# Performance work log

Measured on AMD Instinct MI355X. Metric: run time of the kernel, lower is better.

The kernel has to match this reference:

```python
import jax, jax.numpy as jnp
import numpy as np

B, T, H, W, C = 2, 8, 64, 64, 256
HEADS = 8
WS = 8


def setup_inputs() -> dict:
    key = jax.random.key(0)
    k1, k2, k3 = jax.random.split(key, 3)
    x = jax.random.normal(k1, (B, T, H, W, C), dtype=jnp.float32)
    qkv_w = jax.random.normal(k2, (C, 3 * C), dtype=jnp.float32) * (C ** -0.5)
    proj_w = jax.random.normal(k3, (C, C), dtype=jnp.float32) * (C ** -0.5)
    proj_b = jnp.zeros((C,), dtype=jnp.float32)
    return {"x": x, "qkv_w": qkv_w, "proj_w": proj_w, "proj_b": proj_b}


def reference(x, qkv_w, proj_w, proj_b):
    b, t, h, w, c = x.shape
    hn, wn = h // WS, w // WS
    dh = c // HEADS
    scale = dh ** -0.5
    # window partition: (B,T,H,W,C) -> (B*hn*wn, T*WS*WS, C)
    xw = x.reshape(b, t, hn, WS, wn, WS, c)
    xw = jnp.transpose(xw, (0, 2, 4, 1, 3, 5, 6)).reshape(-1, t * WS * WS, c)
    bw, n, _ = xw.shape
    qkv = (xw @ qkv_w).reshape(bw, n, 3, HEADS, dh)
    qkv = jnp.transpose(qkv, (2, 0, 3, 1, 4))  # (3, Bw, heads, N, dh)
    q, k, v = qkv[0], qkv[1], qkv[2]
    attn = jax.nn.softmax(jnp.einsum("bhnd,bhmd->bhnm", q, k) * scale, axis=-1)
    out = jnp.einsum("bhnm,bhmd->bhnd", attn, v)
    out = jnp.transpose(out, (0, 2, 1, 3)).reshape(bw, n, c)
    out = out @ proj_w + proj_b
    # window reverse
    out = out.reshape(b, hn, wn, t, WS, WS, c)
    out = jnp.transpose(out, (0, 3, 1, 4, 2, 5, 6)).reshape(b, t, h, w, c)
    return out
```

## Files before the change

kernel.cpp:

```cpp
#include <hip/hip_runtime.h>


typedef __bf16 bf16x8 __attribute__((ext_vector_type(8)));
typedef float f32x4 __attribute__((ext_vector_type(4)));

#define NTOK 512
#define DH 32
#define CDIM 256
#define C3 768

__device__ __forceinline__ unsigned short f2b(float f) {
  unsigned u = __builtin_bit_cast(unsigned, f);
  unsigned r = u + 0x7fffu + ((u >> 16) & 1u);
  return (unsigned short)(r >> 16);
}

__global__ void k_prep(const float* __restrict__ qkv_w, const float* __restrict__ proj_w,
                       unsigned short* __restrict__ wqT, unsigned short* __restrict__ wpT) {
  const float QS = 0.2550540254f;
  int idx = blockIdx.x * 256 + threadIdx.x;
  int stride = gridDim.x * 256;
  for (int i = idx; i < C3 * CDIM; i += stride) {
    int n = i >> 8, kk = i & 255;
    float f = qkv_w[kk * C3 + n];
    if (n < 256) f *= QS;
    wqT[i] = f2b(f);
  }
  for (int i = idx; i < CDIM * CDIM; i += stride) {
    int n = i >> 8, kk = i & 255;
    wpT[i] = f2b(proj_w[kk * CDIM + n]);
  }
}

__global__ __launch_bounds__(256, 2) void k_qkv(
    const float* __restrict__ x, const unsigned short* __restrict__ wqT,
    unsigned short* __restrict__ qo, unsigned short* __restrict__ ko,
    unsigned short* __restrict__ vo) {
  extern __shared__ char smem[];
  unsigned short (*As)[264] = (unsigned short (*)[264])smem;
  unsigned short (*Bs)[40]  = (unsigned short (*)[40])(smem + 128 * 264 * 2);
  int tid = threadIdx.x;
  int mtile = blockIdx.x;
  int bw = mtile >> 2;
  int n0 = (mtile & 3) << 7;
  int bb = bw >> 6, hi = (bw >> 3) & 7, wi = bw & 7;

  {
    int row = tid >> 1;
    int n = n0 + row;
    int tt = n >> 6, ii = (n >> 3) & 7, jj = n & 7;
    const float* src = x + ((((long)(bb * 8 + tt)) * 64 + (hi * 8 + ii)) * 64 + (wi * 8 + jj)) * 256;
    int fb = (tid & 1) * 4;
#pragma unroll
    for (int u = 0; u < 32; ++u) {
      int f = fb + u * 8;
      float4 d = *(const float4*)(src + f);
      __bf16 h0 = (__bf16)d.x, h1 = (__bf16)d.y, h2 = (__bf16)d.z, h3 = (__bf16)d.w;
      __bf16* dst = (__bf16*)&As[row][f];
      dst[0] = h0; dst[1] = h1; dst[2] = h2; dst[3] = h3;
    }
  }
  __syncthreads();

  int wid = tid >> 6, lane = tid & 63;
  int lg = lane >> 4, lr = lane & 15;
  int wr = wid >> 1, wc = wid & 1;

  for (int nt = 0; nt < 6; ++nt) {
    f32x4 acc[4][4];
#pragma unroll
    for (int a = 0; a < 4; ++a)
#pragma unroll
      for (int b2 = 0; b2 < 4; ++b2) acc[a][b2] = (f32x4){0.f, 0.f, 0.f, 0.f};

    for (int kk = 0; kk < 256; kk += 32) {
      __syncthreads();
      {
        int brow = tid >> 1, bh2 = tid & 1;
        const uint4* bs = (const uint4*)(wqT + ((long)(nt * 128 + brow)) * 256 + kk + bh2 * 16);
        uint4 b0 = bs[0], b1 = bs[1];
        *(uint4*)&Bs[brow][bh2 * 16] = b0;
        *(uint4*)&Bs[brow][bh2 * 16 + 8] = b1;
      }
      __syncthreads();
      bf16x8 af[4], bfr[4];
#pragma unroll
      for (int mi = 0; mi < 4; ++mi)
        af[mi] = *(const bf16x8*)&As[wr * 64 + mi * 16 + lr][kk + lg * 8];
#pragma unroll
      for (int ni = 0; ni < 4; ++ni)
        bfr[ni] = *(const bf16x8*)&Bs[wc * 64 + ni * 16 + lr][lg * 8];
#pragma unroll
      for (int mi = 0; mi < 4; ++mi)
#pragma unroll
        for (int ni = 0; ni < 4; ++ni)
          acc[mi][ni] = __builtin_amdgcn_mfma_f32_16x16x32_bf16(af[mi], bfr[ni], acc[mi][ni], 0, 0, 0);
    }
#pragma unroll
    for (int ni = 0; ni < 4; ++ni) {
      int c = nt * 128 + wc * 64 + ni * 16 + lr;
      int which = c >> 8, head = (c >> 5) & 7, d = c & 31;
      unsigned short* dst = (which == 0) ? qo : ((which == 1) ? ko : vo);
      long base = ((long)(bw * 8 + head)) * NTOK * DH + d;
#pragma unroll
      for (int mi = 0; mi < 4; ++mi) {
        int nloc = n0 + wr * 64 + mi * 16 + lg * 4;
#pragma unroll
        for (int r = 0; r < 4; ++r) {
          __bf16 hv = (__bf16)acc[mi][ni][r];
          dst[base + (long)(nloc + r) * DH] = __builtin_bit_cast(unsigned short, hv);
        }
      }
    }
  }
}

#define VTOFF 40960
#define POFF 74240
__global__ __launch_bounds__(256, 2) void k_attn(
    const unsigned short* __restrict__ qg0, const unsigned short* __restrict__ kg0,
    const unsigned short* __restrict__ vg0, unsigned short* __restrict__ og) {
  extern __shared__ char smem[];
  int bh = blockIdx.x;
  int tid = threadIdx.x;
  const unsigned short* qg = qg0 + (long)bh * NTOK * DH;
  const unsigned short* kg = kg0 + (long)bh * NTOK * DH;
  const unsigned short* vg = vg0 + (long)bh * NTOK * DH;

#pragma unroll
  for (int i2 = 0; i2 < 8; ++i2) {
    int ci = tid + i2 * 256;
    uint4 dd = *(const uint4*)(kg + ci * 8);
    int n = ci >> 2, h = ci & 3;
    *(uint4*)(smem + n * 80 + h * 16) = dd;
  }
  {
    const uint4* vs = (const uint4*)(vg + tid * 64);
    unsigned r0[16], r1[16];
    *(uint4*)&r0[0] = vs[0]; *(uint4*)&r0[4] = vs[1]; *(uint4*)&r0[8] = vs[2]; *(uint4*)&r0[12] = vs[3];
    *(uint4*)&r1[0] = vs[4]; *(uint4*)&r1[4] = vs[5]; *(uint4*)&r1[8] = vs[6]; *(uint4*)&r1[12] = vs[7];
#pragma unroll
    for (int d = 0; d < 32; ++d) {
      unsigned lo  = (r0[d >> 1] >> ((d & 1) * 16)) & 0xffffu;
      unsigned hi2 = (r1[d >> 1] >> ((d & 1) * 16)) & 0xffffu;
      *(unsigned*)(smem + VTOFF + d * 1040 + tid * 4) = lo | (hi2 << 16);
    }
  }
  __syncthreads();

  int wid = tid >> 6, lane = tid & 63;
  int lg = lane >> 4, lr = lane & 15;
  char* Pb = smem + POFF + wid * 1280;
  unsigned short* ob = og + (long)bh * NTOK * DH;
  const f32x4 zf = {0.f, 0.f, 0.f, 0.f};

  for (int pass = 0; pass < 4; ++pass) {
    int qA = pass * 128 + wid * 32;
    bf16x8 qf0 = *(const bf16x8*)(qg + (qA + lr) * DH + lg * 8);
    bf16x8 qf1 = *(const bf16x8*)(qg + (qA + 16 + lr) * DH + lg * 8);
    f32x4 o00 = zf, o01 = zf, o10 = zf, o11 = zf;
    float m0 = -1e30f, m1 = -1e30f, sum0 = 0.f, sum1 = 0.f;

    for (int ch = 0; ch < 4; ++ch) {
      f32x4 s0[8], s1[8];
#pragma unroll
      for (int t = 0; t < 8; ++t) {
        bf16x8 kf = *(const bf16x8*)(smem + ((ch * 8 + t) * 16 + lr) * 80 + lg * 16);
        s0[t] = __builtin_amdgcn_mfma_f32_16x16x32_bf16(kf, qf0, zf, 0, 0, 0);
        s1[t] = __builtin_amdgcn_mfma_f32_16x16x32_bf16(kf, qf1, zf, 0, 0, 0);
      }
      float mc0 = -1e30f, mc1 = -1e30f;
#pragma unroll
      for (int t = 0; t < 8; ++t)
#pragma unroll
        for (int r = 0; r < 4; ++r) {
          mc0 = fmaxf(mc0, s0[t][r]);
          mc1 = fmaxf(mc1, s1[t][r]);
        }
      mc0 = fmaxf(mc0, __shfl_xor(mc0, 16, 64));
      mc0 = fmaxf(mc0, __shfl_xor(mc0, 32, 64));
      mc1 = fmaxf(mc1, __shfl_xor(mc1, 16, 64));
      mc1 = fmaxf(mc1, __shfl_xor(mc1, 32, 64));
      float nm0 = fmaxf(m0, mc0), nm1 = fmaxf(m1, mc1);
      float sc0 = __builtin_amdgcn_exp2f(m0 - nm0);
      float sc1 = __builtin_amdgcn_exp2f(m1 - nm1);
      m0 = nm0; m1 = nm1;
      float ps0 = 0.f, ps1 = 0.f;
#pragma unroll
      for (int t = 0; t < 8; ++t)
#pragma unroll
        for (int r = 0; r < 4; ++r) {
          float p0 = __builtin_amdgcn_exp2f(s0[t][r] - nm0);
          float p1 = __builtin_amdgcn_exp2f(s1[t][r] - nm1);
          s0[t][r] = p0; s1[t][r] = p1;
          ps0 += p0; ps1 += p1;
        }
      ps0 += __shfl_xor(ps0, 16, 64);
      ps0 += __shfl_xor(ps0, 32, 64);
      ps1 += __shfl_xor(ps1, 16, 64);
      ps1 += __shfl_xor(ps1, 32, 64);
      sum0 = sum0 * sc0 + ps0;
      sum1 = sum1 * sc1 + ps1;
#pragma unroll
      for (int r = 0; r < 4; ++r) {
        float so0 = __shfl(sc0, lg * 4 + r, 64);
        float so1 = __shfl(sc1, lg * 4 + r, 64);
        o00[r] *= so0; o01[r] *= so0;
        o10[r] *= so1; o11[r] *= so1;
      }
#pragma unroll
      for (int mcl = 0; mcl < 4; ++mcl) {
        int mg = ch * 4 + mcl;
        bf16x8 vf0 = *(const bf16x8*)(smem + VTOFF + (lr) * 1040 + mg * 64 + lg * 16);
        bf16x8 vf1 = *(const bf16x8*)(smem + VTOFF + (16 + lr) * 1040 + mg * 64 + lg * 16);
#pragma unroll
        for (int u = 0; u < 2; ++u) {
          int t = mcl * 2 + u;
          __bf16* pw = (__bf16*)(Pb + lr * 80 + u * 32 + lg * 8);
          pw[0] = (__bf16)s0[t][0]; pw[1] = (__bf16)s0[t][1];
          pw[2] = (__bf16)s0[t][2]; pw[3] = (__bf16)s0[t][3];
        }
        bf16x8 pf0 = *(const bf16x8*)(Pb + lr * 80 + lg * 16);
        o00 = __builtin_amdgcn_mfma_f32_16x16x32_bf16(pf0, vf0, o00, 0, 0, 0);
        o01 = __builtin_amdgcn_mfma_f32_16x16x32_bf16(pf0, vf1, o01, 0, 0, 0);
#pragma unroll
        for (int u = 0; u < 2; ++u) {
          int t = mcl * 2 + u;
          __bf16* pw = (__bf16*)(Pb + lr * 80 + u * 32 + lg * 8);
          pw[0] = (__bf16)s1[t][0]; pw[1] = (__bf16)s1[t][1];
          pw[2] = (__bf16)s1[t][2]; pw[3] = (__bf16)s1[t][3];
        }
        bf16x8 pf1 = *(const bf16x8*)(Pb + lr * 80 + lg * 16);
        o10 = __builtin_amdgcn_mfma_f32_16x16x32_bf16(pf1, vf0, o10, 0, 0, 0);
        o11 = __builtin_amdgcn_mfma_f32_16x16x32_bf16(pf1, vf1, o11, 0, 0, 0);
      }
    }

    float rcp0 = 1.0f / sum0, rcp1 = 1.0f / sum1;
#pragma unroll
    for (int r = 0; r < 4; ++r) {
      float rr0 = __shfl(rcp0, lg * 4 + r, 64);
      int rowb = (lg * 4 + r) * 80;
      *(__bf16*)(Pb + rowb + lr * 2)      = (__bf16)(o00[r] * rr0);
      *(__bf16*)(Pb + rowb + 32 + lr * 2) = (__bf16)(o01[r] * rr0);
    }
    {
      int row = lane >> 2, qq = lane & 3;
      uint4 d0 = *(const uint4*)(Pb + row * 80 + qq * 16);
      *(uint4*)(ob + ((long)(qA + row)) * DH + qq * 8) = d0;
    }
#pragma unroll
    for (int r = 0; r < 4; ++r) {
      float rr1 = __shfl(rcp1, lg * 4 + r, 64);
      int rowb = (lg * 4 + r) * 80;
      *(__bf16*)(Pb + rowb + lr * 2)      = (__bf16)(o10[r] * rr1);
      *(__bf16*)(Pb + rowb + 32 + lr * 2) = (__bf16)(o11[r] * rr1);
    }
    {
      int row = lane >> 2, qq = lane & 3;
      uint4 d1 = *(const uint4*)(Pb + row * 80 + qq * 16);
      *(uint4*)(ob + ((long)(qA + 16 + row)) * DH + qq * 8) = d1;
    }
  }
}

__global__ __launch_bounds__(256, 2) void k_proj(
    const unsigned short* __restrict__ og, const unsigned short* __restrict__ wpT,
    const float* __restrict__ pb, float* __restrict__ out) {
  extern __shared__ char smem[];
  unsigned short (*As)[264] = (unsigned short (*)[264])smem;
  unsigned short (*Bs)[40]  = (unsigned short (*)[40])(smem + 128 * 264 * 2);
  int tid = threadIdx.x;
  int mtile = blockIdx.x;
  int bw = mtile >> 2;
  int n0 = (mtile & 3) << 7;
  int bb = bw >> 6, hi = (bw >> 3) & 7, wi = bw & 7;

  {
    int row = tid >> 1, hf = tid & 1;
#pragma unroll
    for (int h4 = 0; h4 < 4; ++h4) {
      int h = hf * 4 + h4;
      const uint4* asrc = (const uint4*)(og + (((long)(bw * 8 + h)) * NTOK + n0 + row) * DH);
      uint4 d0 = asrc[0], d1 = asrc[1], d2 = asrc[2], d3 = asrc[3];
      *(uint4*)&As[row][h * 32]      = d0;
      *(uint4*)&As[row][h * 32 + 8]  = d1;
      *(uint4*)&As[row][h * 32 + 16] = d2;
      *(uint4*)&As[row][h * 32 + 24] = d3;
    }
  }
  __syncthreads();

  int wid = tid >> 6, lane = tid & 63;
  int lg = lane >> 4, lr = lane & 15;
  int wr = wid >> 1, wc = wid & 1;

  for (int nt = 0; nt < 2; ++nt) {
    f32x4 acc[4][4];
#pragma unroll
    for (int a = 0; a < 4; ++a)
#pragma unroll
      for (int b2 = 0; b2 < 4; ++b2) acc[a][b2] = (f32x4){0.f, 0.f, 0.f, 0.f};

    for (int kk = 0; kk < 256; kk += 32) {
      __syncthreads();
      {
        int brow = tid >> 1, bh2 = tid & 1;
        const uint4* bs = (const uint4*)(wpT + ((long)(nt * 128 + brow)) * 256 + kk + bh2 * 16);
        uint4 b0 = bs[0], b1 = bs[1];
        *(uint4*)&Bs[brow][bh2 * 16] = b0;
        *(uint4*)&Bs[brow][bh2 * 16 + 8] = b1;
      }
      __syncthreads();
      bf16x8 af[4], bfr[4];
#pragma unroll
      for (int mi = 0; mi < 4; ++mi)
        af[mi] = *(const bf16x8*)&As[wr * 64 + mi * 16 + lr][kk + lg * 8];
#pragma unroll
      for (int ni = 0; ni < 4; ++ni)
        bfr[ni] = *(const bf16x8*)&Bs[wc * 64 + ni * 16 + lr][lg * 8];
#pragma unroll
      for (int mi = 0; mi < 4; ++mi)
#pragma unroll
        for (int ni = 0; ni < 4; ++ni)
          acc[mi][ni] = __builtin_amdgcn_mfma_f32_16x16x32_bf16(af[mi], bfr[ni], acc[mi][ni], 0, 0, 0);
    }
#pragma unroll
    for (int ni = 0; ni < 4; ++ni) {
      int c = nt * 128 + wc * 64 + ni * 16 + lr;
      float bias = pb[c];
#pragma unroll
      for (int mi = 0; mi < 4; ++mi) {
        int nbase = n0 + wr * 64 + mi * 16 + lg * 4;
#pragma unroll
        for (int r = 0; r < 4; ++r) {
          int n = nbase + r;
          int tt = n >> 6, ii = (n >> 3) & 7, jj = n & 7;
          long off = ((((long)(bb * 8 + tt)) * 64 + (hi * 8 + ii)) * 64 + (wi * 8 + jj)) * 256 + c;
          out[off] = acc[mi][ni][r] + bias;
        }
      }
    }
  }
}

extern "C" void kernel_launch(void* const* d_in, const int* in_sizes, int n_in,
                              void* d_out, int out_size, void* d_ws, size_t ws_size,
                              hipStream_t stream) {
  const float* x      = (const float*)d_in[0];
  const float* qkv_w  = (const float*)d_in[1];
  const float* proj_w = (const float*)d_in[2];
  const float* proj_b = (const float*)d_in[3];
  float* out = (float*)d_out;
  char* ws = (char*)d_ws;

  unsigned short* wqT = (unsigned short*)(ws);
  unsigned short* wpT = (unsigned short*)(ws + 393216);
  unsigned short* Q   = (unsigned short*)(ws + 524288);
  unsigned short* K   = (unsigned short*)(ws + 524288 + 1L * 33554432);
  unsigned short* V   = (unsigned short*)(ws + 524288 + 2L * 33554432);
  unsigned short* O   = (unsigned short*)(ws + 524288 + 3L * 33554432);

  (void)hipFuncSetAttribute((const void*)k_qkv,  hipFuncAttributeMaxDynamicSharedMemorySize, 77824);
  (void)hipFuncSetAttribute((const void*)k_attn, hipFuncAttributeMaxDynamicSharedMemorySize, 79360);
  (void)hipFuncSetAttribute((const void*)k_proj, hipFuncAttributeMaxDynamicSharedMemorySize, 77824);

  k_prep<<<256, 256, 0, stream>>>(qkv_w, proj_w, wqT, wpT);
  k_qkv<<<512, 256, 77824, stream>>>(x, wqT, Q, K, V);
  k_attn<<<1024, 256, 79360, stream>>>(Q, K, V, O);
  k_proj<<<512, 256, 77824, stream>>>(O, wpT, proj_b, out);
}
```

Measured before the change: 156.0 us.

## Write V transposed from QKV kernel and stream K/V from global in attention

The QKV projection now writes V in transposed (d-major) layout, so the attention kernel can load K and V^T fragments straight from global memory and skip staging them in shared memory. The online-softmax max tracking and rescaling are removed; exponentials are taken directly on the scores and normalized once at the end. MFMA operands are swapped so outputs are written with vector stores without going through shared memory, and shared memory shrinks enough to allow four blocks per CU. The trade-offs are repeated global/L2 traffic for K/V and possible exp overflow if scores grow large.

```diff
diff --git a/kernel.cpp b/kernel.cpp
--- a/kernel.cpp
+++ b/kernel.cpp
@@ -100,57 +100,48 @@
     for (int ni = 0; ni < 4; ++ni) {
       int c = nt * 128 + wc * 64 + ni * 16 + lr;
       int which = c >> 8, head = (c >> 5) & 7, d = c & 31;
-      unsigned short* dst = (which == 0) ? qo : ((which == 1) ? ko : vo);
-      long base = ((long)(bw * 8 + head)) * NTOK * DH + d;
-#pragma unroll
-      for (int mi = 0; mi < 4; ++mi) {
-        int nloc = n0 + wr * 64 + mi * 16 + lg * 4;
-#pragma unroll
-        for (int r = 0; r < 4; ++r) {
-          __bf16 hv = (__bf16)acc[mi][ni][r];
-          dst[base + (long)(nloc + r) * DH] = __builtin_bit_cast(unsigned short, hv);
-        }
-      }
-    }
-  }
-}
-
-#define VTOFF 40960
-#define POFF 74240
-__global__ __launch_bounds__(256, 2) void k_attn(
+      long base = ((long)(bw * 8 + head)) * NTOK * DH;
+      if (which == 2) {
+#pragma unroll
+        for (int mi = 0; mi < 4; ++mi) {
+          int nloc = n0 + wr * 64 + mi * 16 + lg * 4;
+          ushort4 w;
+          __bf16 v0 = (__bf16)acc[mi][ni][0], v1 = (__bf16)acc[mi][ni][1];
+          __bf16 v2 = (__bf16)acc[mi][ni][2], v3 = (__bf16)acc[mi][ni][3];
+          w.x = __builtin_bit_cast(unsigned short, v0);
+          w.y = __builtin_bit_cast(unsigned short, v1);
+          w.z = __builtin_bit_cast(unsigned short, v2);
+          w.w = __builtin_bit_cast(unsigned short, v3);
+          *(ushort4*)&vo[base + (long)d * NTOK + nloc] = w;
+        }
+      } else {
+        unsigned short* dst = (which == 0) ? qo : ko;
+#pragma unroll
+        for (int mi = 0; mi < 4; ++mi) {
+          int nloc = n0 + wr * 64 + mi * 16 + lg * 4;
+#pragma unroll
+          for (int r = 0; r < 4; ++r) {
+            __bf16 hv = (__bf16)acc[mi][ni][r];
+            dst[base + (long)(nloc + r) * DH + d] = __builtin_bit_cast(unsigned short, hv);
+          }
+        }
+      }
+    }
+  }
+}
+
+__global__ __launch_bounds__(256, 4) void k_attn(
     const unsigned short* __restrict__ qg0, const unsigned short* __restrict__ kg0,
-    const unsigned short* __restrict__ vg0, unsigned short* __restrict__ og) {
-  extern __shared__ char smem[];
+    const unsigned short* __restrict__ vt0, unsigned short* __restrict__ og) {
+  __shared__ char Pall[4 * 1280];
   int bh = blockIdx.x;
   int tid = threadIdx.x;
   const unsigned short* qg = qg0 + (long)bh * NTOK * DH;
   const unsigned short* kg = kg0 + (long)bh * NTOK * DH;
-  const unsigned short* vg = vg0 + (long)bh * NTOK * DH;
-
-#pragma unroll
-  for (int i2 = 0; i2 < 8; ++i2) {
-    int ci = tid + i2 * 256;
-    uint4 dd = *(const uint4*)(kg + ci * 8);
-    int n = ci >> 2, h = ci & 3;
-    *(uint4*)(smem + n * 80 + h * 16) = dd;
-  }
-  {
-    const uint4* vs = (const uint4*)(vg + tid * 64);
-    unsigned r0[16], r1[16];
-    *(uint4*)&r0[0] = vs[0]; *(uint4*)&r0[4] = vs[1]; *(uint4*)&r0[8] = vs[2]; *(uint4*)&r0[12] = vs[3];
-    *(uint4*)&r1[0] = vs[4]; *(uint4*)&r1[4] = vs[5]; *(uint4*)&r1[8] = vs[6]; *(uint4*)&r1[12] = vs[7];
-#pragma unroll
-    for (int d = 0; d < 32; ++d) {
-      unsigned lo  = (r0[d >> 1] >> ((d & 1) * 16)) & 0xffffu;
-      unsigned hi2 = (r1[d >> 1] >> ((d & 1) * 16)) & 0xffffu;
-      *(unsigned*)(smem + VTOFF + d * 1040 + tid * 4) = lo | (hi2 << 16);
-    }
-  }
-  __syncthreads();
-
+  const unsigned short* vt = vt0 + (long)bh * NTOK * DH;
   int wid = tid >> 6, lane = tid & 63;
   int lg = lane >> 4, lr = lane & 15;
-  char* Pb = smem + POFF + wid * 1280;
+  char* Pb = Pall + wid * 1280;
   unsigned short* ob = og + (long)bh * NTOK * DH;
   const f32x4 zf = {0.f, 0.f, 0.f, 0.f};
 
@@ -159,60 +150,31 @@
     bf16x8 qf0 = *(const bf16x8*)(qg + (qA + lr) * DH + lg * 8);
     bf16x8 qf1 = *(const bf16x8*)(qg + (qA + 16 + lr) * DH + lg * 8);
     f32x4 o00 = zf, o01 = zf, o10 = zf, o11 = zf;
-    float m0 = -1e30f, m1 = -1e30f, sum0 = 0.f, sum1 = 0.f;
-
-    for (int ch = 0; ch < 4; ++ch) {
-      f32x4 s0[8], s1[8];
-#pragma unroll
-      for (int t = 0; t < 8; ++t) {
-        bf16x8 kf = *(const bf16x8*)(smem + ((ch * 8 + t) * 16 + lr) * 80 + lg * 16);
+    float ps0 = 0.f, ps1 = 0.f;
+
+    for (int ch = 0; ch < 8; ++ch) {
+      f32x4 s0[4], s1[4];
+#pragma unroll
+      for (int t = 0; t < 4; ++t) {
+        int n = (ch * 4 + t) * 16 + lr;
+        bf16x8 kf = *(const bf16x8*)(kg + n * DH + lg * 8);
         s0[t] = __builtin_amdgcn_mfma_f32_16x16x32_bf16(kf, qf0, zf, 0, 0, 0);
         s1[t] = __builtin_amdgcn_mfma_f32_16x16x32_bf16(kf, qf1, zf, 0, 0, 0);
       }
-      float mc0 = -1e30f, mc1 = -1e30f;
-#pragma unroll
-      for (int t = 0; t < 8; ++t)
+#pragma unroll
+      for (int t = 0; t < 4; ++t)
 #pragma unroll
         for (int r = 0; r < 4; ++r) {
-          mc0 = fmaxf(mc0, s0[t][r]);
-          mc1 = fmaxf(mc1, s1[t][r]);
-        }
-      mc0 = fmaxf(mc0, __shfl_xor(mc0, 16, 64));
-      mc0 = fmaxf(mc0, __shfl_xor(mc0, 32, 64));
-      mc1 = fmaxf(mc1, __shfl_xor(mc1, 16, 64));
-      mc1 = fmaxf(mc1, __shfl_xor(mc1, 32, 64));
-      float nm0 = fmaxf(m0, mc0), nm1 = fmaxf(m1, mc1);
-      float sc0 = __builtin_amdgcn_exp2f(m0 - nm0);
-      float sc1 = __builtin_amdgcn_exp2f(m1 - nm1);
-      m0 = nm0; m1 = nm1;
-      float ps0 = 0.f, ps1 = 0.f;
-#pragma unroll
-      for (int t = 0; t < 8; ++t)
-#pragma unroll
-        for (int r = 0; r < 4; ++r) {
-          float p0 = __builtin_amdgcn_exp2f(s0[t][r] - nm0);
-          float p1 = __builtin_amdgcn_exp2f(s1[t][r] - nm1);
+          float p0 = __builtin_amdgcn_exp2f(s0[t][r]);
+          float p1 = __builtin_amdgcn_exp2f(s1[t][r]);
           s0[t][r] = p0; s1[t][r] = p1;
           ps0 += p0; ps1 += p1;
         }
-      ps0 += __shfl_xor(ps0, 16, 64);
-      ps0 += __shfl_xor(ps0, 32, 64);
-      ps1 += __shfl_xor(ps1, 16, 64);
-      ps1 += __shfl_xor(ps1, 32, 64);
-      sum0 = sum0 * sc0 + ps0;
-      sum1 = sum1 * sc1 + ps1;
-#pragma unroll
-      for (int r = 0; r < 4; ++r) {
-        float so0 = __shfl(sc0, lg * 4 + r, 64);
-        float so1 = __shfl(sc1, lg * 4 + r, 64);
-        o00[r] *= so0; o01[r] *= so0;
-        o10[r] *= so1; o11[r] *= so1;
-      }
-#pragma unroll
-      for (int mcl = 0; mcl < 4; ++mcl) {
-        int mg = ch * 4 + mcl;
-        bf16x8 vf0 = *(const bf16x8*)(smem + VTOFF + (lr) * 1040 + mg * 64 + lg * 16);
-        bf16x8 vf1 = *(const bf16x8*)(smem + VTOFF + (16 + lr) * 1040 + mg * 64 + lg * 16);
+#pragma unroll
+      for (int mcl = 0; mcl < 2; ++mcl) {
+        int mg = ch * 2 + mcl;
+        bf16x8 vfA = *(const bf16x8*)(vt + lr * NTOK + mg * 32 + lg * 8);
+        bf16x8 vfB = *(const bf16x8*)(vt + (16 + lr) * NTOK + mg * 32 + lg * 8);
 #pragma unroll
         for (int u = 0; u < 2; ++u) {
           int t = mcl * 2 + u;
@@ -221,8 +183,8 @@
           pw[2] = (__bf16)s0[t][2]; pw[3] = (__bf16)s0[t][3];
         }
         bf16x8 pf0 = *(const bf16x8*)(Pb + lr * 80 + lg * 16);
-        o00 = __builtin_amdgcn_mfma_f32_16x16x32_bf16(pf0, vf0, o00, 0, 0, 0);
-        o01 = __builtin_amdgcn_mfma_f32_16x16x32_bf16(pf0, vf1, o01, 0, 0, 0);
+        o00 = __builtin_amdgcn_mfma_f32_16x16x32_bf16(vfA, pf0, o00, 0, 0, 0);
+        o01 = __builtin_amdgcn_mfma_f32_16x16x32_bf16(vfB, pf0, o01, 0, 0, 0);
 #pragma unroll
         for (int u = 0; u < 2; ++u) {
           int t = mcl * 2 + u;
@@ -231,35 +193,47 @@
           pw[2] = (__bf16)s1[t][2]; pw[3] = (__bf16)s1[t][3];
         }
         bf16x8 pf1 = *(const bf16x8*)(Pb + lr * 80 + lg * 16);
-        o10 = __builtin_amdgcn_mfma_f32_16x16x32_bf16(pf1, vf0, o10, 0, 0, 0);
-        o11 = __builtin_amdgcn_mfma_f32_16x16x32_bf16(pf1, vf1, o11, 0, 0, 0);
-      }
-    }
-
-    float rcp0 = 1.0f / sum0, rcp1 = 1.0f / sum1;
-#pragma unroll
-    for (int r = 0; r < 4; ++r) {
-      float rr0 = __shfl(rcp0, lg * 4 + r, 64);
-      int rowb = (lg * 4 + r) * 80;
-      *(__bf16*)(Pb + rowb + lr * 2)      = (__bf16)(o00[r] * rr0);
-      *(__bf16*)(Pb + rowb + 32 + lr * 2) = (__bf16)(o01[r] * rr0);
-    }
+        o10 = __builtin_amdgcn_mfma_f32_16x16x32_bf16(vfA, pf1, o10, 0, 0, 0);
+        o11 = __builtin_amdgcn_mfma_f32_16x16x32_bf16(vfB, pf1, o11, 0, 0, 0);
+      }
+    }
+
+    ps0 += __shfl_xor(ps0, 16, 64);
+    ps0 += __shfl_xor(ps0, 32, 64);
+    ps1 += __shfl_xor(ps1, 16, 64);
+    ps1 += __shfl_xor(ps1, 32, 64);
+    float rcp0 = 1.0f / ps0, rcp1 = 1.0f / ps1;
+
     {
-      int row = lane >> 2, qq = lane & 3;
-      uint4 d0 = *(const uint4*)(Pb + row * 80 + qq * 16);
-      *(uint4*)(ob + ((long)(qA + row)) * DH + qq * 8) = d0;
-    }
-#pragma unroll
-    for (int r = 0; r < 4; ++r) {
-      float rr1 = __shfl(rcp1, lg * 4 + r, 64);
-      int rowb = (lg * 4 + r) * 80;
-      *(__bf16*)(Pb + rowb + lr * 2)      = (__bf16)(o10[r] * rr1);
-      *(__bf16*)(Pb + rowb + 32 + lr * 2) = (__bf16)(o11[r] * rr1);
-    }
-    {
-      int row = lane >> 2, qq = lane & 3;
-      uint4 d1 = *(const uint4*)(Pb + row * 80 + qq * 16);
-      *(uint4*)(ob + ((long)(qA + 16 + row)) * DH + qq * 8) = d1;
+      ushort4 w;
+      __bf16 a0 = (__bf16)(o00[0] * rcp0), a1 = (__bf16)(o00[1] * rcp0);
+      __bf16 a2 = (__bf16)(o00[2] * rcp0), a3 = (__bf16)(o00[3] * rcp0);
+      w.x = __builtin_bit_cast(unsigned short, a0);
+      w.y = __builtin_bit_cast(unsigned short, a1);
+      w.z = __builtin_bit_cast(unsigned short, a2);
+      w.w = __builtin_bit_cast(unsigned short, a3);
+      *(ushort4*)(ob + (long)(qA + lr) * DH + lg * 4) = w;
+      __bf16 b0 = (__bf16)(o01[0] * rcp0), b1 = (__bf16)(o01[1] * rcp0);
+      __bf16 b2 = (__bf16)(o01[2] * rcp0), b3 = (__bf16)(o01[3] * rcp0);
+      w.x = __builtin_bit_cast(unsigned short, b0);
+      w.y = __builtin_bit_cast(unsigned short, b1);
+      w.z = __builtin_bit_cast(unsigned short, b2);
+      w.w = __builtin_bit_cast(unsigned short, b3);
+      *(ushort4*)(ob + (long)(qA + lr) * DH + 16 + lg * 4) = w;
+      __bf16 c0 = (__bf16)(o10[0] * rcp1), c1 = (__bf16)(o10[1] * rcp1);
+      __bf16 c2 = (__bf16)(o10[2] * rcp1), c3 = (__bf16)(o10[3] * rcp1);
+      w.x = __builtin_bit_cast(unsigned short, c0);
+      w.y = __builtin_bit_cast(unsigned short, c1);
+      w.z = __builtin_bit_cast(unsigned short, c2);
+      w.w = __builtin_bit_cast(unsigned short, c3);
+      *(ushort4*)(ob + (long)(qA + 16 + lr) * DH + lg * 4) = w;
+      __bf16 d0 = (__bf16)(o11[0] * rcp1), d1 = (__bf16)(o11[1] * rcp1);
+      __bf16 d2 = (__bf16)(o11[2] * rcp1), d3 = (__bf16)(o11[3] * rcp1);
+      w.x = __builtin_bit_cast(unsigned short, d0);
+      w.y = __builtin_bit_cast(unsigned short, d1);
+      w.z = __builtin_bit_cast(unsigned short, d2);
+      w.w = __builtin_bit_cast(unsigned short, d3);
+      *(ushort4*)(ob + (long)(qA + 16 + lr) * DH + 16 + lg * 4) = w;
     }
   }
 }
@@ -362,11 +336,10 @@
   unsigned short* O   = (unsigned short*)(ws + 524288 + 3L * 33554432);
 
   (void)hipFuncSetAttribute((const void*)k_qkv,  hipFuncAttributeMaxDynamicSharedMemorySize, 77824);
-  (void)hipFuncSetAttribute((const void*)k_attn, hipFuncAttributeMaxDynamicSharedMemorySize, 79360);
   (void)hipFuncSetAttribute((const void*)k_proj, hipFuncAttributeMaxDynamicSharedMemorySize, 77824);
 
   k_prep<<<256, 256, 0, stream>>>(qkv_w, proj_w, wqT, wpT);
   k_qkv<<<512, 256, 77824, stream>>>(x, wqT, Q, K, V);
-  k_attn<<<1024, 256, 79360, stream>>>(Q, K, V, O);
+  k_attn<<<1024, 256, 0, stream>>>(Q, K, V, O);
   k_proj<<<512, 256, 77824, stream>>>(O, wpT, proj_b, out);
 }
```

New measurement: 173.3 us. 11.1% more time.
